# Optimization experiments

Measured on AMD Instinct MI355X. Metric: run time of the kernel, lower is better.

Reference implementation:

```python
import jax, jax.numpy as jnp
import numpy as np

NUM_USER = 50000
NUM_ITEM = 50000
NUM_NODES = NUM_USER + NUM_ITEM
DIM_LATENT = 256
DIM_ID = 64
NUM_EDGES = 2_000_000


def setup_inputs() -> dict:
    key = jax.random.key(0)
    ks = jax.random.split(key, 16)
    xn = lambda k, shape, s: (jax.random.normal(k, shape, dtype=jnp.float32) * s)
    # xavier-normal-ish std for [in,out] weights
    def xavier(k, fan_in, fan_out):
        std = float(np.sqrt(2.0 / (fan_in + fan_out)))
        return jax.random.normal(k, (fan_in, fan_out), dtype=jnp.float32) * std
    edge_index = jax.random.randint(ks[0], (2, NUM_EDGES), 0, NUM_NODES, dtype=jnp.int64)
    return {
        "features": xn(ks[1], (NUM_ITEM, DIM_LATENT), 1.0),
        "id_embedding": xn(ks[2], (NUM_NODES, DIM_ID), 1.0),
        "preference": xn(ks[3], (NUM_USER, DIM_LATENT), 0.1),
        "W_gcn0": xavier(ks[4], DIM_LATENT, DIM_ID),
        "W_gcn1": xavier(ks[5], DIM_ID, DIM_ID),
        "lin_w0": xavier(ks[6], DIM_LATENT, DIM_ID),
        "lin_b0": jnp.zeros((DIM_ID,), jnp.float32),
        "lin_w1": xavier(ks[7], DIM_ID, DIM_ID),
        "lin_b1": jnp.zeros((DIM_ID,), jnp.float32),
        "g_w0": xavier(ks[8], DIM_ID, DIM_ID),
        "g_b0": jnp.zeros((DIM_ID,), jnp.float32),
        "g_w1": xavier(ks[9], DIM_ID, DIM_ID),
        "g_b1": jnp.zeros((DIM_ID,), jnp.float32),
        "edge_index": edge_index,
    }


def _gcn(x, W, row, col, norm):
    # H = scatter_add(row, (x W)[col] * norm)
    h = x @ W                                  # [N, out]
    msg = h[col] * norm[:, None]               # [E, out] gather + scale
    return jax.ops.segment_sum(msg, row, num_segments=NUM_NODES)


def reference(features, id_embedding, preference, W_gcn0, W_gcn1,
              lin_w0, lin_b0, lin_w1, lin_b1, g_w0, g_b0, g_w1, g_b1,
              edge_index):
    row, col = edge_index[0], edge_index[1]
    # degree normalization: deg from scatter_add of ones over row
    deg = jax.ops.segment_sum(jnp.ones((row.shape[0],), jnp.float32), row,
                              num_segments=NUM_NODES)
    deg = jnp.maximum(deg, 1.0)
    dis = deg ** -0.5
    norm = dis[row] * dis[col]                 # [E]

    x = jnp.concatenate([preference, features], axis=0)   # [N, dim_latent]
    x = x / jnp.maximum(jnp.linalg.norm(x, axis=1, keepdims=True), 1e-12)

    lrelu = jax.nn.leaky_relu  # slope 0.01, matches torch default
    for W_gcn, lin_w, lin_b, g_w, g_b in (
        (W_gcn0, lin_w0, lin_b0, g_w0, g_b0),
        (W_gcn1, lin_w1, lin_b1, g_w1, g_b1),
    ):
        h = lrelu(_gcn(x, W_gcn, row, col, norm))          # [N, dim_id]
        x_hat = lrelu(x @ lin_w + lin_b) + id_embedding    # has_id=True
        x = lrelu(h @ g_w + g_b + x_hat)                   # concate=False
    return x
```

## Files before the change

### kernel.cpp

```cpp
#include <hip/hip_runtime.h>

#define NUM_USER   50000
#define NUM_ITEM   50000
#define NUM_NODES  100000
#define DIM_LATENT 256
#define DIM_ID     64
#define NUM_EDGES  2000000
#define NBUCKET    391
#define BPB        4096
#define NCHUNK     489
#define HSTRIDE    392
#define MAXBKT     8192
#define ZROW       NUM_NODES

typedef __attribute__((ext_vector_type(8))) short bf8_t;
typedef __attribute__((ext_vector_type(4))) float f4_t;
typedef __attribute__((ext_vector_type(2))) float f2_t;

static __device__ __forceinline__ float lrelu(float x) {
    return x > 0.0f ? x : 0.01f * x;
}
static __device__ __forceinline__ unsigned short f2bf(float f) {
    unsigned u = __float_as_uint(f);
    u += 0x7fff + ((u >> 16) & 1);
    return (unsigned short)(u >> 16);
}
static __device__ __forceinline__ unsigned cvtpk_bf16(float lo, float hi) {
    unsigned r;
    asm("v_cvt_pk_bf16_f32 %0, %1, %2" : "=v"(r) : "v"(lo), "v"(hi));
    return r;
}
static __device__ __forceinline__ float bf2f(unsigned short u) {
    return __uint_as_float(((unsigned)u) << 16);
}
static __device__ __forceinline__ float bflo(unsigned u) {
    return __uint_as_float(u << 16);
}
static __device__ __forceinline__ float bfhi(unsigned u) {
    return __uint_as_float(u & 0xffff0000u);
}
static __device__ __forceinline__ f2_t shfl2(f2_t v, int off) {
    long long l = __shfl_xor(__builtin_bit_cast(long long, v), off);
    return __builtin_bit_cast(f2_t, l);
}

__global__ void __launch_bounds__(256, 8) k_xnorm(const float* __restrict__ pref,
                                                  const float* __restrict__ feat,
                                                  unsigned short* __restrict__ xn,
                                                  unsigned* __restrict__ hbf8z) {
    if (blockIdx.x == 0 && threadIdx.x < 16)
        hbf8z[(size_t)ZROW * 16 + threadIdx.x] = 0u;
    const int w = threadIdx.x >> 6;
    const int lane = threadIdx.x & 63;
    const int n0 = blockIdx.x * 8 + w * 2;
    const float* s0 = (n0 < NUM_USER) ? (pref + (size_t)n0 * DIM_LATENT)
                                      : (feat + (size_t)(n0 - NUM_USER) * DIM_LATENT);
    const int n1 = n0 + 1;
    const float* s1 = (n1 < NUM_USER) ? (pref + (size_t)n1 * DIM_LATENT)
                                      : (feat + (size_t)(n1 - NUM_USER) * DIM_LATENT);
    float4 v0 = reinterpret_cast<const float4*>(s0)[lane];
    float4 v1 = reinterpret_cast<const float4*>(s1)[lane];
    float a = v0.x*v0.x + v0.y*v0.y + v0.z*v0.z + v0.w*v0.w;
    float b = v1.x*v1.x + v1.y*v1.y + v1.z*v1.z + v1.w*v1.w;
    #pragma unroll
    for (int off = 32; off >= 1; off >>= 1) {
        a += __shfl_xor(a, off);
        b += __shfl_xor(b, off);
    }
    float c0 = 1.0f / fmaxf(sqrtf(a), 1e-12f);
    float c1 = 1.0f / fmaxf(sqrtf(b), 1e-12f);
    uint2 p0, p1;
    p0.x = cvtpk_bf16(v0.x * c0, v0.y * c0);
    p0.y = cvtpk_bf16(v0.z * c0, v0.w * c0);
    p1.x = cvtpk_bf16(v1.x * c1, v1.y * c1);
    p1.y = cvtpk_bf16(v1.z * c1, v1.w * c1);
    *reinterpret_cast<uint2*>(&xn[(size_t)n0 * DIM_LATENT + lane * 4]) = p0;
    *reinterpret_cast<uint2*>(&xn[(size_t)n1 * DIM_LATENT + lane * 4]) = p1;
}

__global__ void __launch_bounds__(256) k_hist(const int* __restrict__ row,
                                              int* __restrict__ hist) {
    __shared__ int lh[NBUCKET];
    const int g = blockIdx.x, t = threadIdx.x;
    for (int i = t; i < NBUCKET; i += 256) lh[i] = 0;
    __syncthreads();
    const int base = g * BPB;
    for (int i = 0; i < BPB; i += 256) {
        int e = base + i + t;
        if (e < NUM_EDGES) atomicAdd(&lh[row[e] >> 8], 1);
    }
    __syncthreads();
    for (int i = t; i < NBUCKET; i += 256) hist[g * HSTRIDE + i] = lh[i];
}

__global__ void __launch_bounds__(512) k_off1(int* __restrict__ hist,
                                              int* __restrict__ bcnt) {
    __shared__ int wsum[8];
    const int b = blockIdx.x, t = threadIdx.x;
    const int lane = t & 63, w = t >> 6;
    int c = (t < NCHUNK) ? hist[t * HSTRIDE + b] : 0;
    int v = c;
    #pragma unroll
    for (int off = 1; off < 64; off <<= 1) {
        int u = __shfl_up(v, off);
        if (lane >= off) v += u;
    }
    if (lane == 63) wsum[w] = v;
    __syncthreads();
    int add = 0;
    #pragma unroll
    for (int i = 0; i < 8; ++i) if (i < w) add += wsum[i];
    int incl = v + add;
    if (t < NCHUNK) hist[t * HSTRIDE + b] = incl - c;
    if (t == 511) bcnt[b] = incl;
}

__global__ void __launch_bounds__(512) k_bscan(const int* __restrict__ bcnt,
                                               int* __restrict__ boff) {
    __shared__ int wsum[8];
    const int t = threadIdx.x;
    const int lane = t & 63, w = t >> 6;
    int c = (t < NBUCKET) ? bcnt[t] : 0;
    int v = c;
    #pragma unroll
    for (int off = 1; off < 64; off <<= 1) {
        int u = __shfl_up(v, off);
        if (lane >= off) v += u;
    }
    if (lane == 63) wsum[w] = v;
    __syncthreads();
    int add = 0;
    #pragma unroll
    for (int i = 0; i < 8; ++i) if (i < w) add += wsum[i];
    int ex = v + add - c;
    if (t < NBUCKET) boff[t] = ex;
    if (t == NBUCKET - 1) boff[NBUCKET] = ex + c;
}

__global__ void __launch_bounds__(256) k_bin2(const int* __restrict__ row,
                                              const int* __restrict__ col,
                                              const int* __restrict__ hist,
                                              const int* __restrict__ boff,
                                              unsigned* __restrict__ epk) {
    __shared__ int curs[NBUCKET];
    const int g = blockIdx.x, t = threadIdx.x;
    for (int i = t; i < NBUCKET; i += 256) curs[i] = boff[i] + hist[g * HSTRIDE + i];
    __syncthreads();
    const int base = g * BPB;
    for (int i = 0; i < BPB; i += 256) {
        int e = base + i + t;
        if (e < NUM_EDGES) {
            int r = row[e];
            int pos = atomicAdd(&curs[r >> 8], 1);
            epk[pos] = ((unsigned)(r & 255) << 24) | (unsigned)col[e];
        }
    }
}

__global__ void __launch_bounds__(512) k_csr(unsigned* __restrict__ epk,
                                             const int* __restrict__ boff,
                                             int* __restrict__ offs,
                                             int* __restrict__ cnt,
                                             float* __restrict__ dis) {
    __shared__ unsigned stage[MAXBKT];
    __shared__ int lcnt[256];
    __shared__ int lofs[256];
    __shared__ int wsum[4];
    const int b = blockIdx.x, t = threadIdx.x;
    const int start = boff[b];
    int m = boff[b + 1] - start;
    if (m > MAXBKT) m = MAXBKT;

    if (t < 256) lcnt[t] = 0;
    for (int e = t; e < m; e += 512) stage[e] = epk[start + e];
    __syncthreads();
    for (int e = t; e < m; e += 512) atomicAdd(&lcnt[stage[e] >> 24], 1);
    __syncthreads();

    const int lane = t & 63, w = t >> 6;
    int c = (t < 256) ? lcnt[t] : 0;
    int v = c;
    #pragma unroll
    for (int off = 1; off < 64; off <<= 1) {
        int u = __shfl_up(v, off);
        if (lane >= off) v += u;
    }
    if (t < 256 && lane == 63) wsum[w] = v;
    __syncthreads();
    if (t < 256) {
        int add = 0;
        #pragma unroll
        for (int i = 0; i < 4; ++i) if (i < w) add += wsum[i];
        int ex = v + add - c;
        lofs[t] = start + ex;
        int n = (b << 8) + t;
        if (n < NUM_NODES) {
            offs[n] = start + ex;
            cnt[n]  = c;
            dis[n]  = rsqrtf((float)max(c, 1));
        }
    }
    __syncthreads();
    for (int e = t; e < m; e += 512) {
        unsigned p = stage[e];
        int pos = atomicAdd(&lofs[p >> 24], 1);
        epk[pos] = p & 0x00ffffffu;
    }
}

__global__ void __launch_bounds__(256) k_wprep(const float* __restrict__ Wg,
                                               const float* __restrict__ Wl,
                                               unsigned short* __restrict__ wfrag) {
    int g = blockIdx.x * 256 + threadIdx.x;
    if (g >= 4096) return;
    int ks = g >> 9;
    int t  = (g >> 6) & 7;
    int l  = g & 63;
    const float* W = (t < 4) ? Wg : Wl;
    int colg = (t & 3) * 16 + (l & 15);
    int kb = ks * 32 + (l >> 4) * 8;
    unsigned short o[8];
    #pragma unroll
    for (int e = 0; e < 8; ++e) o[e] = f2bf(W[(size_t)(kb + e) * DIM_ID + colg]);
    unsigned short* dst = wfrag + (size_t)g * 8;
    #pragma unroll
    for (int e = 0; e < 8; ++e) dst[e] = o[e];
}

__global__ void __launch_bounds__(256) k_wprep64(const float* __restrict__ W0,
                                                 const float* __restrict__ W1,
                                                 const float* __restrict__ W2,
                                                 const float* __restrict__ W3,
                                                 unsigned short* __restrict__ frag) {
    int g = blockIdx.x * 256 + threadIdx.x;
    if (g >= 2048) return;
    int m = g >> 9;
    int r = g & 511;
    int ks = r >> 8;
    int t  = (r >> 6) & 3;
    int l  = r & 63;
    const float* W = (m == 0) ? W0 : (m == 1) ? W1 : (m == 2) ? W2 : W3;
    int colg = t * 16 + (l & 15);
    int kb = ks * 32 + (l >> 4) * 8;
    unsigned short o[8];
    #pragma unroll
    for (int e = 0; e < 8; ++e) o[e] = f2bf(W[(size_t)(kb + e) * DIM_ID + colg]);
    unsigned short* dst = frag + (size_t)g * 8;
    #pragma unroll
    for (int e = 0; e < 8; ++e) dst[e] = o[e];
}

__global__ void __launch_bounds__(256, 3) k_l1(
    const unsigned short* __restrict__ xn,
    const unsigned short* __restrict__ wfrag,
    const float* __restrict__ lb,   const float* __restrict__ idemb,
    const float* __restrict__ dis,
    unsigned char* __restrict__ hbf8, unsigned short* __restrict__ xhat)
{
    __shared__ unsigned short st[4][16][68];
    const int lane = threadIdx.x & 63;
    const int w = threadIdx.x >> 6;
    const int ql = lane & 15, q = lane >> 4;
    const int rowBase = (blockIdx.x * 4 + w) * 16;
    const int rown = rowBase + ql;
    const unsigned short* src = xn + (size_t)((rown < NUM_NODES) ? rown : 0) * DIM_LATENT;

    bf8_t af[8];
    #pragma unroll
    for (int ks = 0; ks < 8; ++ks)
        af[ks] = *reinterpret_cast<const bf8_t*>(src + ks * 32 + q * 8);

    f4_t acc[8];
    #pragma unroll
    for (int t = 0; t < 8; ++t) acc[t] = (f4_t){0.f, 0.f, 0.f, 0.f};

    const bf8_t* wf = reinterpret_cast<const bf8_t*>(wfrag);
    #pragma unroll
    for (int ks = 0; ks < 8; ++ks) {
        #pragma unroll
        for (int t = 0; t < 8; ++t) {
            bf8_t b = wf[(ks * 8 + t) * 64 + lane];
            acc[t] = __builtin_amdgcn_mfma_f32_16x16x32_bf16(af[ks], b, acc[t], 0, 0, 0);
        }
    }

    int nn[4];
    float dn[4];
    #pragma unroll
    for (int reg = 0; reg < 4; ++reg) {
        nn[reg] = rowBase + q * 4 + reg;
        dn[reg] = (nn[reg] < NUM_NODES) ? dis[nn[reg]] : 0.0f;
    }

    #pragma unroll
    for (int t = 0; t < 4; ++t)
        #pragma unroll
        for (int reg = 0; reg < 4; ++reg)
            st[w][q * 4 + reg][t * 16 + ql] = f2bf(acc[t][reg] * dn[reg]);
    #pragma unroll
    for (int it = 0; it < 4; ++it) {
        int i = it * 64 + lane;
        int r = i >> 4, c8 = i & 15;
        int n = rowBase + r;
        uint2 s = *reinterpret_cast<const uint2*>(&st[w][r][c8 * 4]);
        if (n < NUM_NODES) {
            int p = __builtin_amdgcn_cvt_pk_fp8_f32(bflo(s.x), bfhi(s.x), 0, false);
            p = __builtin_amdgcn_cvt_pk_fp8_f32(bflo(s.y), bfhi(s.y), p, true);
            *reinterpret_cast<unsigned*>(hbf8 + (size_t)n * DIM_ID + c8 * 4) = (unsigned)p;
        }
    }

    #pragma unroll
    for (int t = 4; t < 8; ++t) {
        int colg = (t - 4) * 16 + ql;
        float lbl = lb[colg];
        #pragma unroll
        for (int reg = 0; reg < 4; ++reg)
            st[w][q * 4 + reg][colg] = f2bf(lrelu(acc[t][reg] + lbl));
    }
    #pragma unroll
    for (int it = 0; it < 4; ++it) {
        int i = it * 64 + lane;
        int r = i >> 4, c8 = i & 15;
        int n = rowBase + r;
        if (n < NUM_NODES) {
            uint2 s = *reinterpret_cast<const uint2*>(&st[w][r][c8 * 4]);
            float4 idv = *reinterpret_cast<const float4*>(&idemb[(size_t)n * DIM_ID + c8 * 4]);
            uint2 o;
            o.x = (unsigned)f2bf(bflo(s.x) + idv.x) | ((unsigned)f2bf(bfhi(s.x) + idv.y) << 16);
            o.y = (unsigned)f2bf(bflo(s.y) + idv.z) | ((unsigned)f2bf(bfhi(s.y) + idv.w) << 16);
            *reinterpret_cast<uint2*>(&xhat[(size_t)n * DIM_ID + c8 * 4]) = o;
        }
    }
}

__global__ void __launch_bounds__(256, 8) k_gather(
    const unsigned char* __restrict__ hbf8, const float* __restrict__ dis,
    const int* __restrict__ offs, const int* __restrict__ cnt,
    const int* __restrict__ ecol, unsigned short* __restrict__ Hb)
{
    const int w = threadIdx.x >> 6;
    const int lane = threadIdx.x & 63;
    const int g = lane >> 3;
    const int k = lane & 7;
    const int n = blockIdx.x * 4 + w;

    const float dn = dis[n];
    const int start = offs[n];
    const int m = cnt[n];

    f2_t s01 = {0.f, 0.f}, s23 = {0.f, 0.f}, s45 = {0.f, 0.f}, s67 = {0.f, 0.f};

    for (int base = 0; base < m; base += 64) {
        int e = base + lane;
        int ec = (e < m) ? ecol[start + e] : ZROW;
        int lim = m - base; if (lim > 64) lim = 64;
        int ns = (lim + 31) >> 5;
        for (int s = 0; s < ns; ++s) {
            int i0 = s * 32 + g;
            int c0 = __shfl(ec, i0);
            int c1 = __shfl(ec, i0 + 8);
            int c2 = __shfl(ec, i0 + 16);
            int c3 = __shfl(ec, i0 + 24);
            uint2 u0 = *reinterpret_cast<const uint2*>(hbf8 + (size_t)(c0 << 6) + (k << 3));
            uint2 u1 = *reinterpret_cast<const uint2*>(hbf8 + (size_t)(c1 << 6) + (k << 3));
            uint2 u2 = *reinterpret_cast<const uint2*>(hbf8 + (size_t)(c2 << 6) + (k << 3));
            uint2 u3 = *reinterpret_cast<const uint2*>(hbf8 + (size_t)(c3 << 6) + (k << 3));
            s01 += __builtin_amdgcn_cvt_pk_f32_fp8(u0.x, false);
            s23 += __builtin_amdgcn_cvt_pk_f32_fp8(u0.x, true);
            s45 += __builtin_amdgcn_cvt_pk_f32_fp8(u0.y, false);
            s67 += __builtin_amdgcn_cvt_pk_f32_fp8(u0.y, true);
            s01 += __builtin_amdgcn_cvt_pk_f32_fp8(u1.x, false);
            s23 += __builtin_amdgcn_cvt_pk_f32_fp8(u1.x, true);
            s45 += __builtin_amdgcn_cvt_pk_f32_fp8(u1.y, false);
            s67 += __builtin_amdgcn_cvt_pk_f32_fp8(u1.y, true);
            s01 += __builtin_amdgcn_cvt_pk_f32_fp8(u2.x, false);
            s23 += __builtin_amdgcn_cvt_pk_f32_fp8(u2.x, true);
            s45 += __builtin_amdgcn_cvt_pk_f32_fp8(u2.y, false);
            s67 += __builtin_amdgcn_cvt_pk_f32_fp8(u2.y, true);
            s01 += __builtin_amdgcn_cvt_pk_f32_fp8(u3.x, false);
            s23 += __builtin_amdgcn_cvt_pk_f32_fp8(u3.x, true);
            s45 += __builtin_amdgcn_cvt_pk_f32_fp8(u3.y, false);
            s67 += __builtin_amdgcn_cvt_pk_f32_fp8(u3.y, true);
        }
    }
    #pragma unroll
    for (int off = 8; off <= 32; off <<= 1) {
        s01 += shfl2(s01, off);
        s23 += shfl2(s23, off);
        s45 += shfl2(s45, off);
        s67 += shfl2(s67, off);
    }
    if (lane < 8) {
        uint4 o;
        o.x = cvtpk_bf16(s01.x * dn, s01.y * dn);
        o.y = cvtpk_bf16(s23.x * dn, s23.y * dn);
        o.z = cvtpk_bf16(s45.x * dn, s45.y * dn);
        o.w = cvtpk_bf16(s67.x * dn, s67.y * dn);
        *reinterpret_cast<uint4*>(&Hb[(size_t)n * DIM_ID + lane * 8]) = o;
    }
}

__global__ void __launch_bounds__(256, 3) k_mid(
    const unsigned short* __restrict__ Hb, const unsigned short* __restrict__ xhat1,
    const unsigned short* __restrict__ wf64,
    const float* __restrict__ gb,  const float* __restrict__ lb1,
    const float* __restrict__ idemb, const float* __restrict__ dis,
    unsigned char* __restrict__ hbf8, unsigned short* __restrict__ xhat2)
{
    __shared__ unsigned short x1s[4][16][DIM_ID];
    __shared__ unsigned short st[4][16][68];
    const int lane = threadIdx.x & 63;
    const int w = threadIdx.x >> 6;
    const int ql = lane & 15, q = lane >> 4;
    const int rowBase = (blockIdx.x * 4 + w) * 16;
    const int rowc = min(rowBase + ql, NUM_NODES - 1);

    bf8_t ha[2];
    #pragma unroll
    for (int ks = 0; ks < 2; ++ks) {
        uint4 u = *reinterpret_cast<const uint4*>(&Hb[(size_t)rowc * DIM_ID + ks * 32 + q * 8]);
        bf8_t a;
        a[0] = (short)f2bf(lrelu(bflo(u.x))); a[1] = (short)f2bf(lrelu(bfhi(u.x)));
        a[2] = (short)f2bf(lrelu(bflo(u.y))); a[3] = (short)f2bf(lrelu(bfhi(u.y)));
        a[4] = (short)f2bf(lrelu(bflo(u.z))); a[5] = (short)f2bf(lrelu(bfhi(u.z)));
        a[6] = (short)f2bf(lrelu(bflo(u.w))); a[7] = (short)f2bf(lrelu(bfhi(u.w)));
        ha[ks] = a;
    }

    const bf8_t* gw0f = reinterpret_cast<const bf8_t*>(wf64);
    f4_t acc1[4];
    #pragma unroll
    for (int t = 0; t < 4; ++t) acc1[t] = (f4_t){0.f, 0.f, 0.f, 0.f};
    #pragma unroll
    for (int ks = 0; ks < 2; ++ks)
        #pragma unroll
        for (int t = 0; t < 4; ++t)
            acc1[t] = __builtin_amdgcn_mfma_f32_16x16x32_bf16(ha[ks], gw0f[(ks * 4 + t) * 64 + lane], acc1[t], 0, 0, 0);

    int nn[4];
    #pragma unroll
    for (int reg = 0; reg < 4; ++reg) nn[reg] = rowBase + q * 4 + reg;

    #pragma unroll
    for (int t = 0; t < 4; ++t) {
        int colg = t * 16 + ql;
        float gbl = gb[colg];
        #pragma unroll
        for (int reg = 0; reg < 4; ++reg) {
            float xh = bf2f(xhat1[(size_t)min(nn[reg], NUM_NODES - 1) * DIM_ID + colg]);
            x1s[w][q * 4 + reg][colg] = f2bf(lrelu(acc1[t][reg] + gbl + xh));
        }
    }
    __syncthreads();

    bf8_t xa[2];
    #pragma unroll
    for (int ks = 0; ks < 2; ++ks)
        xa[ks] = *reinterpret_cast<const bf8_t*>(&x1s[w][ql][ks * 32 + q * 8]);

    const bf8_t* wg1f = reinterpret_cast<const bf8_t*>(wf64 + 512 * 8);
    const bf8_t* lw1f = reinterpret_cast<const bf8_t*>(wf64 + 1024 * 8);
    f4_t acc2[8];
    #pragma unroll
    for (int t = 0; t < 8; ++t) acc2[t] = (f4_t){0.f, 0.f, 0.f, 0.f};
    #pragma unroll
    for (int ks = 0; ks < 2; ++ks) {
        #pragma unroll
        for (int t = 0; t < 4; ++t)
            acc2[t] = __builtin_amdgcn_mfma_f32_16x16x32_bf16(xa[ks], wg1f[(ks * 4 + t) * 64 + lane], acc2[t], 0, 0, 0);
        #pragma unroll
        for (int t = 0; t < 4; ++t)
            acc2[4 + t] = __builtin_amdgcn_mfma_f32_16x16x32_bf16(xa[ks], lw1f[(ks * 4 + t) * 64 + lane], acc2[4 + t], 0, 0, 0);
    }

    float dn[4];
    #pragma unroll
    for (int reg = 0; reg < 4; ++reg)
        dn[reg] = (nn[reg] < NUM_NODES) ? dis[nn[reg]] : 0.0f;

    #pragma unroll
    for (int t = 0; t < 4; ++t)
        #pragma unroll
        for (int reg = 0; reg < 4; ++reg)
            st[w][q * 4 + reg][t * 16 + ql] = f2bf(acc2[t][reg] * dn[reg]);
    #pragma unroll
    for (int it = 0; it < 4; ++it) {
        int i = it * 64 + lane;
        int r = i >> 4, c8 = i & 15;
        int n = rowBase + r;
        uint2 s = *reinterpret_cast<const uint2*>(&st[w][r][c8 * 4]);
        if (n < NUM_NODES) {
            int p = __builtin_amdgcn_cvt_pk_fp8_f32(bflo(s.x), bfhi(s.x), 0, false);
            p = __builtin_amdgcn_cvt_pk_fp8_f32(bflo(s.y), bfhi(s.y), p, true);
            *reinterpret_cast<unsigned*>(hbf8 + (size_t)n * DIM_ID + c8 * 4) = (unsigned)p;
        }
    }

    #pragma unroll
    for (int t = 0; t < 4; ++t) {
        int colg = t * 16 + ql;
        float lbl = lb1[colg];
        #pragma unroll
        for (int reg = 0; reg < 4; ++reg)
            st[w][q * 4 + reg][colg] = f2bf(lrelu(acc2[4 + t][reg] + lbl));
    }
    #pragma unroll
    for (int it = 0; it < 4; ++it) {
        int i = it * 64 + lane;
        int r = i >> 4, c8 = i & 15;
        int n = rowBase + r;
        if (n < NUM_NODES) {
            uint2 s = *reinterpret_cast<const uint2*>(&st[w][r][c8 * 4]);
            float4 idv = *reinterpret_cast<const float4*>(&idemb[(size_t)n * DIM_ID + c8 * 4]);
            uint2 o;
            o.x = (unsigned)f2bf(bflo(s.x) + idv.x) | ((unsigned)f2bf(bfhi(s.x) + idv.y) << 16);
            o.y = (unsigned)f2bf(bflo(s.y) + idv.z) | ((unsigned)f2bf(bfhi(s.y) + idv.w) << 16);
            *reinterpret_cast<uint2*>(&xhat2[(size_t)n * DIM_ID + c8 * 4]) = o;
        }
    }
}

__global__ void __launch_bounds__(256, 3) k_final(
    const unsigned short* __restrict__ Hb, const unsigned short* __restrict__ xhat,
    const unsigned short* __restrict__ wf64,
    const float* __restrict__ gb, float* __restrict__ out)
{
    const int lane = threadIdx.x & 63;
    const int w = threadIdx.x >> 6;
    const int ql = lane & 15, q = lane >> 4;
    const int rowBase = (blockIdx.x * 4 + w) * 16;
    const int rowc = min(rowBase + ql, NUM_NODES - 1);

    bf8_t ha[2];
    #pragma unroll
    for (int ks = 0; ks < 2; ++ks) {
        uint4 u = *reinterpret_cast<const uint4*>(&Hb[(size_t)rowc * DIM_ID + ks * 32 + q * 8]);
        bf8_t a;
        a[0] = (short)f2bf(lrelu(bflo(u.x))); a[1] = (short)f2bf(lrelu(bfhi(u.x)));
        a[2] = (short)f2bf(lrelu(bflo(u.y))); a[3] = (short)f2bf(lrelu(bfhi(u.y)));
        a[4] = (short)f2bf(lrelu(bflo(u.z))); a[5] = (short)f2bf(lrelu(bfhi(u.z)));
        a[6] = (short)f2bf(lrelu(bflo(u.w))); a[7] = (short)f2bf(lrelu(bfhi(u.w)));
        ha[ks] = a;
    }

    const bf8_t* gw1f = reinterpret_cast<const bf8_t*>(wf64 + 1536 * 8);
    f4_t acc[4];
    #pragma unroll
    for (int t = 0; t < 4; ++t) acc[t] = (f4_t){0.f, 0.f, 0.f, 0.f};
    #pragma unroll
    for (int ks = 0; ks < 2; ++ks)
        #pragma unroll
        for (int t = 0; t < 4; ++t)
            acc[t] = __builtin_amdgcn_mfma_f32_16x16x32_bf16(ha[ks], gw1f[(ks * 4 + t) * 64 + lane], acc[t], 0, 0, 0);

    int nn[4];
    #pragma unroll
    for (int reg = 0; reg < 4; ++reg) nn[reg] = rowBase + q * 4 + reg;

    #pragma unroll
    for (int t = 0; t < 4; ++t) {
        int colg = t * 16 + ql;
        float gbl = gb[colg];
        #pragma unroll
        for (int reg = 0; reg < 4; ++reg)
            if (nn[reg] < NUM_NODES) {
                size_t o = (size_t)nn[reg] * DIM_ID + colg;
                out[o] = lrelu(acc[t][reg] + gbl + bf2f(xhat[o]));
            }
    }
}

extern "C" void kernel_launch(void* const* d_in, const int* in_sizes, int n_in,
                              void* d_out, int out_size, void* d_ws, size_t ws_size,
                              hipStream_t stream)
{
    const float* features = (const float*)d_in[0];
    const float* idemb    = (const float*)d_in[1];
    const float* pref     = (const float*)d_in[2];
    const float* Wg0      = (const float*)d_in[3];
    const float* Wg1      = (const float*)d_in[4];
    const float* lw0      = (const float*)d_in[5];
    const float* lb0      = (const float*)d_in[6];
    const float* lw1      = (const float*)d_in[7];
    const float* lb1      = (const float*)d_in[8];
    const float* gw0      = (const float*)d_in[9];
    const float* gb0      = (const float*)d_in[10];
    const float* gw1      = (const float*)d_in[11];
    const float* gb1      = (const float*)d_in[12];
    const int*   edges    = (const int*)d_in[13];
    const int*   row      = edges;
    const int*   col      = edges + NUM_EDGES;

    char* ws = (char*)d_ws;
    int*      hist  = (int*)(ws + 0);
    int*      bcnt  = (int*)(ws + 1048576);
    int*      boff  = (int*)(ws + 1052672);
    int*      offs  = (int*)(ws + 1056768);
    int*      cnt   = (int*)(ws + 1581056);
    float*    dis   = (float*)(ws + 2105344);
    unsigned short* wfrag = (unsigned short*)(ws + 2629632);
    unsigned short* wf64  = (unsigned short*)(ws + 2695168);
    unsigned short* xn    = (unsigned short*)(ws + 2760704);
    unsigned short* Hbf = (unsigned short*)(ws + 20000000);
    unsigned* epk  = (unsigned*)(ws + 53960704);
    unsigned char*  hbf8  = (unsigned char*)(ws + 62349312);
    unsigned short* xhatb = (unsigned short*)(ws + 68749376);
    float* out   = (float*)d_out;

    const int l1Blocks = (NUM_NODES + 63) / 64;
    const int gatherBlocks = NUM_NODES / 4;

    k_wprep<<<16, 256, 0, stream>>>(Wg0, lw0, wfrag);
    k_wprep64<<<8, 256, 0, stream>>>(gw0, Wg1, lw1, gw1, wf64);

    k_xnorm<<<NUM_NODES / 8, 256, 0, stream>>>(pref, features, xn, (unsigned*)hbf8);
    k_hist<<<NCHUNK, 256, 0, stream>>>(row, hist);
    k_off1<<<NBUCKET, 512, 0, stream>>>(hist, bcnt);
    k_bscan<<<1, 512, 0, stream>>>(bcnt, boff);
    k_bin2<<<NCHUNK, 256, 0, stream>>>(row, col, hist, boff, epk);
    k_csr<<<NBUCKET, 512, 0, stream>>>(epk, boff, offs, cnt, dis);

    k_l1<<<l1Blocks, 256, 0, stream>>>(xn, wfrag, lb0, idemb, dis, hbf8, xhatb);

    k_gather<<<gatherBlocks, 256, 0, stream>>>(hbf8, dis, offs, cnt, (const int*)epk, Hbf);

    k_mid<<<l1Blocks, 256, 0, stream>>>(Hbf, xhatb, wf64, gb0, lb1, idemb, dis,
                                        hbf8, xhatb);

    k_gather<<<gatherBlocks, 256, 0, stream>>>(hbf8, dis, offs, cnt, (const int*)epk, Hbf);
    k_final<<<l1Blocks, 256, 0, stream>>>(Hbf, xhatb, wf64, gb1, out);
}
```

Baseline: 207.4 us.

## Fuse row L2-normalization into first-layer MFMA kernel and drop xnorm pass

Removes the separate normalization kernel that wrote a bf16 copy of the normalized input. The first-layer kernel now reads the fp32 features directly, converts them to bf16 unnormalized, and computes the row sum of squares with shuffles. It then applies the inverse norm to the GEMM outputs, since the row scale commutes with the matmul. This saves a full write and re-read of a 100000x256 bf16 intermediate plus one launch, but the bf16 rounding now happens before scaling, and the fp32 loads inside the MFMA kernel are twice as wide. The zero-row init moves into the weight-prep kernel, and the xhat packing switches to the hardware pack-convert instruction.

```diff
diff --git a/kernel.cpp b/kernel.cpp
--- a/kernel.cpp
+++ b/kernel.cpp
@@ -42,40 +42,6 @@
 static __device__ __forceinline__ f2_t shfl2(f2_t v, int off) {
     long long l = __shfl_xor(__builtin_bit_cast(long long, v), off);
     return __builtin_bit_cast(f2_t, l);
-}
-
-__global__ void __launch_bounds__(256, 8) k_xnorm(const float* __restrict__ pref,
-                                                  const float* __restrict__ feat,
-                                                  unsigned short* __restrict__ xn,
-                                                  unsigned* __restrict__ hbf8z) {
-    if (blockIdx.x == 0 && threadIdx.x < 16)
-        hbf8z[(size_t)ZROW * 16 + threadIdx.x] = 0u;
-    const int w = threadIdx.x >> 6;
-    const int lane = threadIdx.x & 63;
-    const int n0 = blockIdx.x * 8 + w * 2;
-    const float* s0 = (n0 < NUM_USER) ? (pref + (size_t)n0 * DIM_LATENT)
-                                      : (feat + (size_t)(n0 - NUM_USER) * DIM_LATENT);
-    const int n1 = n0 + 1;
-    const float* s1 = (n1 < NUM_USER) ? (pref + (size_t)n1 * DIM_LATENT)
-                                      : (feat + (size_t)(n1 - NUM_USER) * DIM_LATENT);
-    float4 v0 = reinterpret_cast<const float4*>(s0)[lane];
-    float4 v1 = reinterpret_cast<const float4*>(s1)[lane];
-    float a = v0.x*v0.x + v0.y*v0.y + v0.z*v0.z + v0.w*v0.w;
-    float b = v1.x*v1.x + v1.y*v1.y + v1.z*v1.z + v1.w*v1.w;
-    #pragma unroll
-    for (int off = 32; off >= 1; off >>= 1) {
-        a += __shfl_xor(a, off);
-        b += __shfl_xor(b, off);
-    }
-    float c0 = 1.0f / fmaxf(sqrtf(a), 1e-12f);
-    float c1 = 1.0f / fmaxf(sqrtf(b), 1e-12f);
-    uint2 p0, p1;
-    p0.x = cvtpk_bf16(v0.x * c0, v0.y * c0);
-    p0.y = cvtpk_bf16(v0.z * c0, v0.w * c0);
-    p1.x = cvtpk_bf16(v1.x * c1, v1.y * c1);
-    p1.y = cvtpk_bf16(v1.z * c1, v1.w * c1);
-    *reinterpret_cast<uint2*>(&xn[(size_t)n0 * DIM_LATENT + lane * 4]) = p0;
-    *reinterpret_cast<uint2*>(&xn[(size_t)n1 * DIM_LATENT + lane * 4]) = p1;
 }
 
 __global__ void __launch_bounds__(256) k_hist(const int* __restrict__ row,
@@ -210,7 +176,10 @@
 
 __global__ void __launch_bounds__(256) k_wprep(const float* __restrict__ Wg,
                                                const float* __restrict__ Wl,
-                                               unsigned short* __restrict__ wfrag) {
+                                               unsigned short* __restrict__ wfrag,
+                                               unsigned* __restrict__ hbf8z) {
+    if (blockIdx.x == 0 && threadIdx.x < 16)
+        hbf8z[(size_t)ZROW * 16 + threadIdx.x] = 0u;
     int g = blockIdx.x * 256 + threadIdx.x;
     if (g >= 4096) return;
     int ks = g >> 9;
@@ -251,7 +220,7 @@
 }
 
 __global__ void __launch_bounds__(256, 3) k_l1(
-    const unsigned short* __restrict__ xn,
+    const float* __restrict__ pref, const float* __restrict__ feat,
     const unsigned short* __restrict__ wfrag,
     const float* __restrict__ lb,   const float* __restrict__ idemb,
     const float* __restrict__ dis,
@@ -263,12 +232,28 @@
     const int ql = lane & 15, q = lane >> 4;
     const int rowBase = (blockIdx.x * 4 + w) * 16;
     const int rown = rowBase + ql;
-    const unsigned short* src = xn + (size_t)((rown < NUM_NODES) ? rown : 0) * DIM_LATENT;
+    const int rc = (rown < NUM_NODES) ? rown : 0;
+    const float* src = (rc < NUM_USER) ? (pref + (size_t)rc * DIM_LATENT)
+                                       : (feat + (size_t)(rc - NUM_USER) * DIM_LATENT);
 
     bf8_t af[8];
-    #pragma unroll
-    for (int ks = 0; ks < 8; ++ks)
-        af[ks] = *reinterpret_cast<const bf8_t*>(src + ks * 32 + q * 8);
+    float ss = 0.0f;
+    #pragma unroll
+    for (int ks = 0; ks < 8; ++ks) {
+        float4 va = *reinterpret_cast<const float4*>(src + ks * 32 + q * 8);
+        float4 vb = *reinterpret_cast<const float4*>(src + ks * 32 + q * 8 + 4);
+        ss += va.x*va.x + va.y*va.y + va.z*va.z + va.w*va.w
+            + vb.x*vb.x + vb.y*vb.y + vb.z*vb.z + vb.w*vb.w;
+        uint4 au;
+        au.x = cvtpk_bf16(va.x, va.y);
+        au.y = cvtpk_bf16(va.z, va.w);
+        au.z = cvtpk_bf16(vb.x, vb.y);
+        au.w = cvtpk_bf16(vb.z, vb.w);
+        af[ks] = __builtin_bit_cast(bf8_t, au);
+    }
+    ss += __shfl_xor(ss, 16);
+    ss += __shfl_xor(ss, 32);
+    float rn = 1.0f / fmaxf(sqrtf(ss), 1e-12f);
 
     f4_t acc[8];
     #pragma unroll
@@ -284,12 +269,16 @@
         }
     }
 
+    float rn4[4];
+    #pragma unroll
+    for (int reg = 0; reg < 4; ++reg) rn4[reg] = __shfl(rn, q * 4 + reg);
+
     int nn[4];
     float dn[4];
     #pragma unroll
     for (int reg = 0; reg < 4; ++reg) {
         nn[reg] = rowBase + q * 4 + reg;
-        dn[reg] = (nn[reg] < NUM_NODES) ? dis[nn[reg]] : 0.0f;
+        dn[reg] = (nn[reg] < NUM_NODES) ? dis[nn[reg]] * rn4[reg] : 0.0f;
     }
 
     #pragma unroll
@@ -316,7 +305,7 @@
         float lbl = lb[colg];
         #pragma unroll
         for (int reg = 0; reg < 4; ++reg)
-            st[w][q * 4 + reg][colg] = f2bf(lrelu(acc[t][reg] + lbl));
+            st[w][q * 4 + reg][colg] = f2bf(lrelu(acc[t][reg] * rn4[reg] + lbl));
     }
     #pragma unroll
     for (int it = 0; it < 4; ++it) {
@@ -327,8 +316,8 @@
             uint2 s = *reinterpret_cast<const uint2*>(&st[w][r][c8 * 4]);
             float4 idv = *reinterpret_cast<const float4*>(&idemb[(size_t)n * DIM_ID + c8 * 4]);
             uint2 o;
-            o.x = (unsigned)f2bf(bflo(s.x) + idv.x) | ((unsigned)f2bf(bfhi(s.x) + idv.y) << 16);
-            o.y = (unsigned)f2bf(bflo(s.y) + idv.z) | ((unsigned)f2bf(bfhi(s.y) + idv.w) << 16);
+            o.x = cvtpk_bf16(bflo(s.x) + idv.x, bfhi(s.x) + idv.y);
+            o.y = cvtpk_bf16(bflo(s.y) + idv.z, bfhi(s.y) + idv.w);
             *reinterpret_cast<uint2*>(&xhat[(size_t)n * DIM_ID + c8 * 4]) = o;
         }
     }
@@ -514,8 +503,8 @@
             uint2 s = *reinterpret_cast<const uint2*>(&st[w][r][c8 * 4]);
             float4 idv = *reinterpret_cast<const float4*>(&idemb[(size_t)n * DIM_ID + c8 * 4]);
             uint2 o;
-            o.x = (unsigned)f2bf(bflo(s.x) + idv.x) | ((unsigned)f2bf(bfhi(s.x) + idv.y) << 16);
-            o.y = (unsigned)f2bf(bflo(s.y) + idv.z) | ((unsigned)f2bf(bfhi(s.y) + idv.w) << 16);
+            o.x = cvtpk_bf16(bflo(s.x) + idv.x, bfhi(s.x) + idv.y);
+            o.y = cvtpk_bf16(bflo(s.y) + idv.z, bfhi(s.y) + idv.w);
             *reinterpret_cast<uint2*>(&xhat2[(size_t)n * DIM_ID + c8 * 4]) = o;
         }
     }
@@ -601,7 +590,6 @@
     float*    dis   = (float*)(ws + 2105344);
     unsigned short* wfrag = (unsigned short*)(ws + 2629632);
     unsigned short* wf64  = (unsigned short*)(ws + 2695168);
-    unsigned short* xn    = (unsigned short*)(ws + 2760704);
     unsigned short* Hbf = (unsigned short*)(ws + 20000000);
     unsigned* epk  = (unsigned*)(ws + 53960704);
     unsigned char*  hbf8  = (unsigned char*)(ws + 62349312);
@@ -611,17 +599,17 @@
     const int l1Blocks = (NUM_NODES + 63) / 64;
     const int gatherBlocks = NUM_NODES / 4;
 
-    k_wprep<<<16, 256, 0, stream>>>(Wg0, lw0, wfrag);
+    k_wprep<<<16, 256, 0, stream>>>(Wg0, lw0, wfrag, (unsigned*)hbf8);
     k_wprep64<<<8, 256, 0, stream>>>(gw0, Wg1, lw1, gw1, wf64);
 
-    k_xnorm<<<NUM_NODES / 8, 256, 0, stream>>>(pref, features, xn, (unsigned*)hbf8);
     k_hist<<<NCHUNK, 256, 0, stream>>>(row, hist);
     k_off1<<<NBUCKET, 512, 0, stream>>>(hist, bcnt);
     k_bscan<<<1, 512, 0, stream>>>(bcnt, boff);
     k_bin2<<<NCHUNK, 256, 0, stream>>>(row, col, hist, boff, epk);
     k_csr<<<NBUCKET, 512, 0, stream>>>(epk, boff, offs, cnt, dis);
 
-    k_l1<<<l1Blocks, 256, 0, stream>>>(xn, wfrag, lb0, idemb, dis, hbf8, xhatb);
+    k_l1<<<l1Blocks, 256, 0, stream>>>(pref, features, wfrag, lb0, idemb, dis,
+                                       hbf8, xhatb);
 
     k_gather<<<gatherBlocks, 256, 0, stream>>>(hbf8, dis, offs, cnt, (const int*)epk, Hbf);
 
```

Result: faster. 197.4 us (-4.9%).
